# Kernel tuning notes

Measured on AMD Instinct MI355X. Metric: run time of the kernel, lower is better.

Reference implementation:

```python
import jax, jax.numpy as jnp
import numpy as np
from jax import lax

GAMMA = 1.0       # SoftDTW gamma (init default)
MAX_DIST = 10000.0  # clamp in SoftDTW.forward
# bandwidth=None -> 0 -> Sakoe-Chiba pruning disabled (condition 0 < bandwidth never holds)


def _softdtw(D, gamma):
    """Soft-DTW DP via anti-diagonal wavefront scan. D: (B, N, M) -> (B,)."""
    B, N, M = D.shape
    R = jnp.full((B, N + 2, M + 2), jnp.inf, D.dtype).at[:, 0, 0].set(0.0)
    i_vec = jnp.arange(1, N + 1)  # row indices of interior cells

    def step(R, p):
        # cells on anti-diagonal p satisfy i + j == p + 2
        j_vec = p + 2 - i_vec
        valid = (j_vec >= 1) & (j_vec <= M)
        jc = jnp.clip(j_vec, 1, M)
        r0 = R[:, i_vec - 1, jc - 1]  # (B, N) diag
        r1 = R[:, i_vec - 1, jc]      # up
        r2 = R[:, i_vec, jc - 1]      # left
        neg = jnp.stack([r0, r1, r2], axis=0) * (-1.0 / gamma)  # (3, B, N)
        # invalid lanes: keep finite to avoid NaNs (result discarded by where)
        neg = jnp.where(valid[None, None, :], neg, 0.0)
        softmin = -gamma * jax.scipy.special.logsumexp(neg, axis=0)  # (B, N)
        new = D[:, i_vec - 1, jc - 1] + softmin
        R = R.at[:, i_vec, jc].set(jnp.where(valid[None, :], new, R[:, i_vec, jc]))
        return R, None

    R, _ = lax.scan(step, R, jnp.arange(N + M - 1))
    return R[:, N, M]


def setup_inputs() -> dict:
    key = jax.random.key(0)
    kx, ky = jax.random.split(key)
    X = jax.random.normal(kx, (16, 512, 64), dtype=jnp.float32)
    Y = jax.random.normal(ky, (16, 512, 64), dtype=jnp.float32)
    return {"X": X, "Y": Y}


def reference(X, Y):
    # squared Euclidean pairwise distance per timestep (faithful expand form)
    D = jnp.sum((X[:, :, None, :] - Y[:, None, :, :]) ** 2, axis=-1)  # (B, N, M)
    D = jnp.minimum(D, MAX_DIST)
    return _softdtw(D, GAMMA)
```

## Files before the change

### kernel.cpp

```cpp
#include <hip/hip_runtime.h>

#define BIGF 1e30f
#define LOG2E 1.4426950408889634f
#define LN2F 0.6931471805599453f

constexpr int NB = 16;
constexpr int NN = 512;
constexpr int MM = 512;
constexpr int KD = 64;
constexpr int WAVES = 8;
constexpr int CSPAN = 32;
constexpr int NSPANS = 32;
constexpr int SPW = 18;
constexpr int TPH = 3 * (WAVES - 1) + SPW;
constexpr int DIAGELEMS = NN * MM;

constexpr int BBSTRIDE = MM + 2;
constexpr int BUFD_FLOATS = WAVES * 2 * CSPAN * 64;
constexpr int BBUF_FLOATS = WAVES * BBSTRIDE;
constexpr int SMEM_BYTES = (BUFD_FLOATS + BBUF_FLOATS) * 4;

__device__ __forceinline__ int Bclosed(int s) {
  return (s <= 511) ? (s * (s + 1)) / 2
                    : DIAGELEMS - ((1023 - s) * (1024 - s)) / 2 - (s - 511);
}

__global__ __launch_bounds__(256) void pairdist_kernel(
    const float* __restrict__ X, const float* __restrict__ Y,
    float* __restrict__ Dsk) {
  const int b = blockIdx.z;
  const int i0 = blockIdx.y * 64;
  const int j0 = blockIdx.x * 64;

  __shared__ float Xs[64][65];
  __shared__ float Ys[64][65];
  __shared__ float Ds[64][66];

  const float* Xb = X + ((size_t)b * NN + i0) * KD;
  const float* Yb = Y + ((size_t)b * MM + j0) * KD;
  for (int k = threadIdx.x; k < 64 * KD; k += 256) {
    Xs[k >> 6][k & 63] = Xb[k];
    Ys[k >> 6][k & 63] = Yb[k];
  }
  __syncthreads();

  const int tx = threadIdx.x & 15;
  const int ty = threadIdx.x >> 4;
  const int r0 = ty * 4, c0 = tx * 4;

  float acc[4][4];
#pragma unroll
  for (int a = 0; a < 4; ++a)
#pragma unroll
    for (int e = 0; e < 4; ++e) acc[a][e] = 0.0f;

  for (int d = 0; d < KD; ++d) {
    float xv[4], yv[4];
#pragma unroll
    for (int q = 0; q < 4; ++q) xv[q] = Xs[r0 + q][d];
#pragma unroll
    for (int q = 0; q < 4; ++q) yv[q] = Ys[c0 + q][d];
#pragma unroll
    for (int a = 0; a < 4; ++a)
#pragma unroll
      for (int e = 0; e < 4; ++e) {
        float df = xv[a] - yv[e];
        acc[a][e] = fmaf(df, df, acc[a][e]);
      }
  }

#pragma unroll
  for (int a = 0; a < 4; ++a)
#pragma unroll
    for (int e = 0; e < 4; ++e)
      Ds[r0 + a][c0 + e] = fminf(acc[a][e], 10000.0f) * LOG2E;
  __syncthreads();

  const int wv = threadIdx.x >> 6;
  const int ln = threadIdx.x & 63;
  float* Db = Dsk + (size_t)b * DIAGELEMS;
  for (int sl = wv; sl < 127; sl += 4) {
    const int istart = sl > 63 ? sl - 63 : 0;
    const int iend = sl < 63 ? sl : 63;
    if (ln <= iend - istart) {
      const int ig = i0 + istart + ln;
      Db[Bclosed(i0 + j0 + sl) + ig] = Ds[istart + ln][sl - istart - ln];
    }
  }
}

__device__ __forceinline__ float dpp_shr1(float v, float fill) {
  return __int_as_float(__builtin_amdgcn_update_dpp(
      __float_as_int(fill), __float_as_int(v), 0x138 , 0xf, 0xf,
      false));
}

__device__ __forceinline__ void dma_span(const float* __restrict__ Dskb,
                                         float* bufD, int blk, int q,
                                         int lane) {
  float* dst0 = bufD + (blk * 2 + (q & 1)) * (CSPAN * 64);
  const int rbase = 64 * blk + (lane & 15) * 4;
  const int sub = lane >> 4;
#pragma unroll
  for (int u = 0; u < 8; ++u) {
    int s = 32 * q + 4 * u + sub;
    s = s > 1022 ? 1022 : s;
    int e = Bclosed(s) + rbase;
    e = e > DIAGELEMS - 4 ? DIAGELEMS - 4 : e;
    __builtin_amdgcn_global_load_lds(
        (const __attribute__((address_space(1))) void*)(Dskb + e),
        (__attribute__((address_space(3))) void*)(dst0 + u * 256), 16, 0, 0);
  }
}

extern __shared__ float smem[];
__global__ __launch_bounds__(512) void softdtw_kernel(
    const float* __restrict__ Dsk, float* __restrict__ out) {
  const int b = blockIdx.x;
  const int t = threadIdx.x;
  const int wu = __builtin_amdgcn_readfirstlane(t >> 6);
  const int lane = t & 63;
  const int blk = ((wu & 3) << 1) | (wu >> 2);

  float* bufD = smem;
  float* bbuf = smem + BUFD_FLOATS;

  for (int k = t; k < BBUF_FLOATS; k += 512) bbuf[k] = BIGF;
  __syncthreads();

  const float* __restrict__ Dskb = Dsk + (size_t)b * DIAGELEMS;

  dma_span(Dskb, bufD, blk, 2 * blk, lane);

  const int r = 64 * blk + lane;
  float ra = BIGF;
  float up1p = (blk == 0 && lane == 0) ? 0.0f : BIGF;

  for (int S = 0; S < TPH; ++S) {
    const int cc = S - 3 * blk;
    if (cc >= 0 && cc < SPW) {
      const int c = cc + 2 * blk;
      const bool issue = (cc + 1 < SPW);
      if (issue) {
        dma_span(Dskb, bufD, blk, c + 1, lane);
        asm volatile("s_waitcnt vmcnt(8)" ::: "memory");
      } else {
        asm volatile("s_waitcnt vmcnt(0)" ::: "memory");
      }

      int bi = 32 * cc + 1 + (lane & 31);
      bi = bi > 513 ? 513 : bi;
      const float browA = blk ? bbuf[blk * BBSTRIDE + bi] : BIGF;

      const float* myD = bufD + (blk * 2 + (c & 1)) * (CSPAN * 64);
      float dv[CSPAN];
#pragma unroll
      for (int k = 0; k < CSPAN; ++k) dv[k] = myD[k * 64 + lane];

      const int jv0 = 32 * c - r + 1;
#pragma unroll
      for (int k = 0; k < CSPAN; ++k) {
        const float o1 = __int_as_float(
            __builtin_amdgcn_readlane(__float_as_int(browA), k));
        const float up1 = dpp_shr1(ra, o1);
        const float up2 = up1p;
        up1p = up1;

        const float m = fminf(fminf(up1, up2), ra);
        const float md = __builtin_amdgcn_fmed3f(up1, up2, ra);
        const float mx = fmaxf(fmaxf(up1, up2), ra);
        const float ssum = 1.0f + __builtin_amdgcn_exp2f(m - md) +
                           __builtin_amdgcn_exp2f(m - mx);
        const float n = dv[k] + (m - __builtin_amdgcn_logf(ssum));

        const int jv = jv0 + k;
        const bool a0 = (unsigned)(jv - 1) < (unsigned)MM;
        ra = a0 ? n : ra;

        if (blk < WAVES - 1 && lane == 63 && a0)
          bbuf[(blk + 1) * BBSTRIDE + jv] = n;
      }
    }
    __syncthreads();
  }

  if (blk == WAVES - 1 && lane == 63) out[b] = ra * LN2F;
}

extern "C" void kernel_launch(void* const* d_in, const int* in_sizes, int n_in,
                              void* d_out, int out_size, void* d_ws,
                              size_t ws_size, hipStream_t stream) {
  const float* X = (const float*)d_in[0];
  const float* Y = (const float*)d_in[1];
  float* out = (float*)d_out;
  float* Dsk = (float*)d_ws;

  const size_t needed = (size_t)NB * DIAGELEMS * sizeof(float);
  if (ws_size < needed) return;

  hipFuncSetAttribute((const void*)softdtw_kernel,
                      hipFuncAttributeMaxDynamicSharedMemorySize, SMEM_BYTES);

  pairdist_kernel<<<dim3(MM / 64, NN / 64, NB), 256, 0, stream>>>(X, Y, Dsk);
  softdtw_kernel<<<NB, 512, SMEM_BYTES, stream>>>(Dsk, out);
}
```

Before: 148.9 us.

## Use bit-trick exp2/log2, register-prefetched D and DPP-shifted boundary rows in softdtw

The softdtw kernel drops the LDS DMA staging of D and instead prefetches each 32-diagonal span straight from global memory into a register double buffer. The accurate exp2/log hardware calls are replaced with Schraudolph-style bit-manipulation approximations. The upper-boundary value now arrives through a DPP left shift of a per-lane register rather than a readlane. Every lane publishes its value into a padded boundary buffer without a branch, interior phases skip the validity select, and __syncthreads is replaced by lgkmcnt wait plus s_barrier. The aim is to shorten the serial per-cell dependency chain, at the risk of accumulating approximation error across the roughly 1000-step recurrence.

```diff
diff --git a/kernel.cpp b/kernel.cpp
--- a/kernel.cpp
+++ b/kernel.cpp
@@ -15,10 +15,8 @@
 constexpr int TPH = 3 * (WAVES - 1) + SPW;
 constexpr int DIAGELEMS = NN * MM;
 
-constexpr int BBSTRIDE = MM + 2;
-constexpr int BUFD_FLOATS = WAVES * 2 * CSPAN * 64;
+constexpr int BBSTRIDE = 672;
 constexpr int BBUF_FLOATS = WAVES * BBSTRIDE;
-constexpr int SMEM_BYTES = (BUFD_FLOATS + BBUF_FLOATS) * 4;
 
 __device__ __forceinline__ int Bclosed(int s) {
   return (s <= 511) ? (s * (s + 1)) / 2
@@ -89,31 +87,76 @@
   }
 }
 
-__device__ __forceinline__ float dpp_shr1(float v, float fill) {
+__device__ __forceinline__ float dpp_shr1_old(float oldv, float v) {
   return __int_as_float(__builtin_amdgcn_update_dpp(
-      __float_as_int(fill), __float_as_int(v), 0x138 , 0xf, 0xf,
+      __float_as_int(oldv), __float_as_int(v), 0x138 , 0xf, 0xf,
       false));
 }
-
-__device__ __forceinline__ void dma_span(const float* __restrict__ Dskb,
-                                         float* bufD, int blk, int q,
-                                         int lane) {
-  float* dst0 = bufD + (blk * 2 + (q & 1)) * (CSPAN * 64);
-  const int rbase = 64 * blk + (lane & 15) * 4;
-  const int sub = lane >> 4;
-#pragma unroll
-  for (int u = 0; u < 8; ++u) {
-    int s = 32 * q + 4 * u + sub;
-    s = s > 1022 ? 1022 : s;
-    int e = Bclosed(s) + rbase;
-    e = e > DIAGELEMS - 4 ? DIAGELEMS - 4 : e;
-    __builtin_amdgcn_global_load_lds(
-        (const __attribute__((address_space(1))) void*)(Dskb + e),
-        (__attribute__((address_space(3))) void*)(dst0 + u * 256), 16, 0, 0);
-  }
-}
-
-extern __shared__ float smem[];
+__device__ __forceinline__ float dpp_shl1(float v) {
+  return __int_as_float(__builtin_amdgcn_update_dpp(
+      __float_as_int(v), __float_as_int(v), 0x130 , 0xf, 0xf,
+      false));
+}
+
+__device__ __forceinline__ float fexp2(float x) {
+  x = fmaxf(x, -126.0f);
+  return __int_as_float((int)fmaf(x, 8388608.0f, 1.064975338e9f));
+}
+__device__ __forceinline__ float flog2(float y) {
+  return fmaf((float)__float_as_int(y), 1.1920929e-7f, -126.9549534f);
+}
+
+#define FILL(ARR, Q)                                                        \
+  do {                                                                      \
+    const int q_ = (Q);                                                     \
+    int s0_ = 32 * q_;                                                      \
+    int idx_ = Bclosed(s0_ > 1022 ? 1022 : s0_);                            \
+    _Pragma("unroll") for (int k_ = 0; k_ < CSPAN; ++k_) {                  \
+      const int s_ = 32 * q_ + k_;                                          \
+      int e_ = idx_ + r;                                                    \
+      e_ = e_ > DIAGELEMS - 1 ? DIAGELEMS - 1 : e_;                         \
+      ARR[k_] = Du[e_];                                                     \
+      idx_ += (s_ < 511) ? s_ + 1 : ((s_ < 1022) ? 1022 - s_ : 0);          \
+    }                                                                       \
+  } while (0)
+
+#define SOFTMIN_STEP(DVK)                                                   \
+  {                                                                         \
+    const float up1 = dpp_shr1_old(B, ra);                                  \
+    B = dpp_shl1(B);                                                        \
+    const float m = fminf(fminf(up1, up2), ra);                             \
+    const float md = __builtin_amdgcn_fmed3f(up1, up2, ra);                 \
+    const float mx = fmaxf(fmaxf(up1, up2), ra);                            \
+    const float ssum = (fexp2(m - md) + fexp2(m - mx)) + 1.0f;              \
+    n = ((DVK) + m) - flog2(ssum);                                          \
+    up2 = up1;                                                              \
+  }
+
+#define PHASE(DVC, DVN)                                                     \
+  do {                                                                      \
+    if (cc + 1 < SPW) FILL(DVN, c + 1);  \
+    float B = BIGF;                                                         \
+    if (blk) B = bbuf[blk * BBSTRIDE + 62 + 32 * cc + 1 + lane];            \
+    float* pubp =                                                           \
+        bbuf + ((blk + 1) & 7) * BBSTRIDE + (62 + 32 * c - r + 1);          \
+    float n;                                                                \
+    if (cc >= 2 && cc <= 15) {     \
+      _Pragma("unroll") for (int k = 0; k < CSPAN; ++k) {                   \
+        SOFTMIN_STEP(DVC[k]);                                               \
+        ra = n;                                                             \
+        pubp[k] = ra;                                                       \
+      }                                                                     \
+    } else {                           \
+      const int jv0 = 32 * c - r + 1;                                       \
+      _Pragma("unroll") for (int k = 0; k < CSPAN; ++k) {                   \
+        SOFTMIN_STEP(DVC[k]);                                               \
+        const bool a0 = (unsigned)(jv0 + k - 1) < (unsigned)MM;             \
+        ra = a0 ? n : ra;                                                   \
+        pubp[k] = ra;                                                       \
+      }                                                                     \
+    }                                                                       \
+  } while (0)
+
 __global__ __launch_bounds__(512) void softdtw_kernel(
     const float* __restrict__ Dsk, float* __restrict__ out) {
   const int b = blockIdx.x;
@@ -122,66 +165,32 @@
   const int lane = t & 63;
   const int blk = ((wu & 3) << 1) | (wu >> 2);
 
-  float* bufD = smem;
-  float* bbuf = smem + BUFD_FLOATS;
+  __shared__ float bbuf[BBUF_FLOATS];
 
   for (int k = t; k < BBUF_FLOATS; k += 512) bbuf[k] = BIGF;
   __syncthreads();
 
-  const float* __restrict__ Dskb = Dsk + (size_t)b * DIAGELEMS;
-
-  dma_span(Dskb, bufD, blk, 2 * blk, lane);
-
+  const float* __restrict__ Du = Dsk + (size_t)b * DIAGELEMS;
   const int r = 64 * blk + lane;
+
+  float dvA[CSPAN], dvB[CSPAN];
+  FILL(dvA, 2 * blk);
+
   float ra = BIGF;
-  float up1p = (blk == 0 && lane == 0) ? 0.0f : BIGF;
+  float up2 = (blk == 0 && lane == 0) ? 0.0f : BIGF;
 
   for (int S = 0; S < TPH; ++S) {
     const int cc = S - 3 * blk;
     if (cc >= 0 && cc < SPW) {
       const int c = cc + 2 * blk;
-      const bool issue = (cc + 1 < SPW);
-      if (issue) {
-        dma_span(Dskb, bufD, blk, c + 1, lane);
-        asm volatile("s_waitcnt vmcnt(8)" ::: "memory");
+      if (cc & 1) {
+        PHASE(dvB, dvA);
       } else {
-        asm volatile("s_waitcnt vmcnt(0)" ::: "memory");
-      }
-
-      int bi = 32 * cc + 1 + (lane & 31);
-      bi = bi > 513 ? 513 : bi;
-      const float browA = blk ? bbuf[blk * BBSTRIDE + bi] : BIGF;
-
-      const float* myD = bufD + (blk * 2 + (c & 1)) * (CSPAN * 64);
-      float dv[CSPAN];
-#pragma unroll
-      for (int k = 0; k < CSPAN; ++k) dv[k] = myD[k * 64 + lane];
-
-      const int jv0 = 32 * c - r + 1;
-#pragma unroll
-      for (int k = 0; k < CSPAN; ++k) {
-        const float o1 = __int_as_float(
-            __builtin_amdgcn_readlane(__float_as_int(browA), k));
-        const float up1 = dpp_shr1(ra, o1);
-        const float up2 = up1p;
-        up1p = up1;
-
-        const float m = fminf(fminf(up1, up2), ra);
-        const float md = __builtin_amdgcn_fmed3f(up1, up2, ra);
-        const float mx = fmaxf(fmaxf(up1, up2), ra);
-        const float ssum = 1.0f + __builtin_amdgcn_exp2f(m - md) +
-                           __builtin_amdgcn_exp2f(m - mx);
-        const float n = dv[k] + (m - __builtin_amdgcn_logf(ssum));
-
-        const int jv = jv0 + k;
-        const bool a0 = (unsigned)(jv - 1) < (unsigned)MM;
-        ra = a0 ? n : ra;
-
-        if (blk < WAVES - 1 && lane == 63 && a0)
-          bbuf[(blk + 1) * BBSTRIDE + jv] = n;
+        PHASE(dvA, dvB);
       }
     }
-    __syncthreads();
+    asm volatile("s_waitcnt lgkmcnt(0)" ::: "memory");
+    __builtin_amdgcn_s_barrier();
   }
 
   if (blk == WAVES - 1 && lane == 63) out[b] = ra * LN2F;
@@ -198,9 +207,6 @@
   const size_t needed = (size_t)NB * DIAGELEMS * sizeof(float);
   if (ws_size < needed) return;
 
-  hipFuncSetAttribute((const void*)softdtw_kernel,
-                      hipFuncAttributeMaxDynamicSharedMemorySize, SMEM_BYTES);
-
   pairdist_kernel<<<dim3(MM / 64, NN / 64, NB), 256, 0, stream>>>(X, Y, Dsk);
-  softdtw_kernel<<<NB, 512, SMEM_BYTES, stream>>>(Dsk, out);
-}
+  softdtw_kernel<<<NB, 512, 0, stream>>>(Dsk, out);
+}
```

New measurement: 148.1 us. Within noise of the previous version (-0.5%).
